# Kernel optimization log

Measured on AMD Instinct MI355X. Metric: run time of the kernel, lower is better.

Reference implementation:

```python
import jax, jax.numpy as jnp
import numpy as np

N = 1024
NEVAL = 131072
NUM_POLES = 8
DOMAIN = (-1.0, 1.0)
DOMAIN_LEN = DOMAIN[1] - DOMAIN[0]
EPS = 1e-14


def _cheb_nodes(n):
    # Chebyshev points of the second kind: cos(pi * linspace(0, 1, n))
    return jnp.cos(jnp.pi * jnp.linspace(0.0, 1.0, n))


def _to_standard(x):
    return 2.0 * (x - DOMAIN[0]) / DOMAIN_LEN - 1.0


def _barycentric_weights(nodes, poles_real, poles_imag):
    # Vectorized equivalent of the original per-node Python loop.
    n = nodes.shape[0]
    diff = nodes[:, None] - nodes[None, :]            # (N, N)
    eye = jnp.eye(n, dtype=bool)
    # log_weights[j] = -sum_{i!=j} log|nodes[j]-nodes[i]|
    log_w = -jnp.sum(jnp.log(jnp.where(eye, 1.0, jnp.abs(diff))), axis=1)
    # signs[j] = (-1)^(# of negative off-diagonal diffs); diagonal diff==0 contributes nothing
    neg_count = jnp.sum(diff < 0, axis=1)
    signs = jnp.where(neg_count % 2 == 0, 1.0, -1.0)
    # each conjugate pole pair contributes 2*log(sqrt((x-r)^2 + i^2)) = log((x-r)^2 + i^2)
    pole_term = jnp.log((nodes[:, None] - poles_real[None, :]) ** 2
                        + poles_imag[None, :] ** 2)   # (N, M)
    log_w = log_w + jnp.sum(pole_term, axis=1)
    log_w = log_w - jnp.max(log_w)
    w = signs * jnp.exp(log_w)
    return w / jnp.abs(w[0])


def setup_inputs() -> dict:
    key = jax.random.key(0)
    k1, k2, k3, k4 = jax.random.split(key, 4)
    x_eval = jax.random.uniform(k1, (NEVAL,), dtype=jnp.float32)  # in [0,1) subset of domain
    values = jax.random.normal(k2, (N,), dtype=jnp.float32)
    poles_real = jax.random.normal(k3, (NUM_POLES,), dtype=jnp.float32)
    poles_imag = jax.random.normal(k4, (NUM_POLES,), dtype=jnp.float32)
    return {"x_eval": x_eval, "values": values,
            "poles_real": poles_real, "poles_imag": poles_imag}


def reference(x_eval, values, poles_real, poles_imag):
    nodes = _cheb_nodes(N)
    nodes_std = _to_standard(nodes)                   # identity for domain (-1,1)
    w = _barycentric_weights(nodes, poles_real, poles_imag)

    x_std = _to_standard(x_eval)
    d_x = x_std[None, :] - nodes_std[:, None]         # (N, NEVAL)
    small = jnp.abs(d_x) < EPS
    small_any = jnp.any(small, axis=0)                # (NEVAL,)
    d_safe = jnp.where(small, 1.0, d_x)
    inv = jnp.where(small_any[None, :], 0.0, 1.0 / d_safe)
    inv = jnp.where(small, 1.0, inv)                  # exact-hit columns: indicator row -> 1

    num = jnp.einsum('n,nm,n->m', values, inv, w)
    den = jnp.einsum('nm,n->m', inv, w)
    return num / den
```

## Files before the change

kernel.cpp:

```cpp
#include <hip/hip_runtime.h>
#include <math.h>

#define N_NODES 1024
#define N_EVAL 131072
#define NUM_POLES 8
#define PI_D 3.14159265358979323846


__device__ __forceinline__ double cheb_node(int j) {
    return cos(PI_D * (double)j / (double)(N_NODES - 1));
}

__global__ void wk_logw(const float* __restrict__ poles_real,
                        const float* __restrict__ poles_imag,
                        double* __restrict__ lwd) {
    const int j = blockIdx.x;
    const int t = threadIdx.x;
    const double nj = cheb_node(j);
    double part = 0.0;
    for (int i = t; i < N_NODES; i += 256) {
        if (i != j) {
            part -= log(fabs(nj - cheb_node(i)));
        }
    }
    __shared__ double red[256];
    red[t] = part;
    __syncthreads();
    for (int s = 128; s > 0; s >>= 1) {
        if (t < s) red[t] += red[t + s];
        __syncthreads();
    }
    if (t == 0) {
        double lw = red[0];
        for (int m = 0; m < NUM_POLES; ++m) {
            double pr = (double)poles_real[m];
            double pim = (double)poles_imag[m];
            double dr = nj - pr;
            lw += log(dr * dr + pim * pim);
        }
        lwd[j] = lw;
    }
}

__global__ void wk_finalize(const float* __restrict__ values,
                            const double* __restrict__ lwd,
                            float* __restrict__ nodes_f,
                            float* __restrict__ w_f,
                            float* __restrict__ wv_f) {
    const int j = threadIdx.x;
    const double lw = lwd[j];
    __shared__ double red[N_NODES];
    red[j] = lw;
    __syncthreads();
    for (int s = N_NODES / 2; s > 0; s >>= 1) {
        if (j < s) red[j] = fmax(red[j], red[j + s]);
        __syncthreads();
    }
    const double mx = red[0];
    double w = exp(lw - mx);
    if (j & 1) w = -w;
    const float wf = (float)w;
    nodes_f[j] = (float)cheb_node(j);
    w_f[j] = wf;
    wv_f[j] = wf * values[j];
}

__global__ __launch_bounds__(256) void eval_kernel(
    const float* __restrict__ x_eval,
    const float* __restrict__ nodes_f,
    const float* __restrict__ w_f,
    const float* __restrict__ wv_f,
    float* __restrict__ out) {
    __shared__ __align__(16) float s_n[N_NODES];
    __shared__ __align__(16) float s_w[N_NODES];
    __shared__ __align__(16) float s_v[N_NODES];
    const int t = threadIdx.x;
    for (int k = t; k < N_NODES; k += 256) {
        s_n[k] = nodes_f[k];
        s_w[k] = w_f[k];
        s_v[k] = wv_f[k];
    }
    __syncthreads();

    const int i = blockIdx.x * 256 + t;
    const float x = x_eval[i];

    float num = 0.0f, den = 0.0f;
    float hnum = 0.0f, hden = 0.0f;
    bool hit = false;

    const float4* n4 = (const float4*)s_n;
    const float4* w4 = (const float4*)s_w;
    const float4* v4 = (const float4*)s_v;

#define BODY(C)                                                            \
    {                                                                      \
        float d = x - an.C;                                                \
        if (__builtin_expect(fabsf(d) < 1e-14f, 0)) {                      \
            hit = true; hnum += av.C; hden += aw.C;                        \
        } else {                                                           \
            float r = __builtin_amdgcn_rcpf(d);                            \
            r = fmaf(r, fmaf(-d, r, 1.0f), r);          \
            num = fmaf(av.C, r, num);                                      \
            den = fmaf(aw.C, r, den);                                      \
        }                                                                  \
    }

#pragma unroll 4
    for (int j4 = 0; j4 < N_NODES / 4; ++j4) {
        float4 an = n4[j4];
        float4 aw = w4[j4];
        float4 av = v4[j4];
        BODY(x) BODY(y) BODY(z) BODY(w)
    }
#undef BODY

    out[i] = hit ? (hnum / hden) : (num / den);
}

extern "C" void kernel_launch(void* const* d_in, const int* in_sizes, int n_in,
                              void* d_out, int out_size, void* d_ws, size_t ws_size,
                              hipStream_t stream) {
    const float* x_eval     = (const float*)d_in[0];
    const float* values     = (const float*)d_in[1];
    const float* poles_real = (const float*)d_in[2];
    const float* poles_imag = (const float*)d_in[3];
    float* out = (float*)d_out;

    double* lwd    = (double*)d_ws;
    float* nodes_f = (float*)(lwd + N_NODES);
    float* w_f     = nodes_f + N_NODES;
    float* wv_f    = w_f + N_NODES;

    wk_logw<<<N_NODES, 256, 0, stream>>>(poles_real, poles_imag, lwd);
    wk_finalize<<<1, N_NODES, 0, stream>>>(values, lwd, nodes_f, w_f, wv_f);
    eval_kernel<<<N_EVAL / 256, 256, 0, stream>>>(x_eval, nodes_f, w_f, wv_f, out);
}
```

Before: 128.2 us.

## Use closed-form Chebyshev weights and branchless eval with NaN fallback

Replaces the O(N^2) log-sum weight computation and its separate max-reduction kernel with the closed-form Chebyshev second-kind barycentric weights (halved at the endpoints) times the pole product, computed in a single small kernel. The eval loop drops the per-node exact-hit branch, splits accumulation into two chains for more ILP, and only rescans the nodes for an exact match when the result is NaN. Weights are no longer normalised by a max, which risks overflow or scale differences, though these cancel in the ratio.

```diff
diff --git a/kernel.cpp b/kernel.cpp
--- a/kernel.cpp
+++ b/kernel.cpp
@@ -6,63 +6,26 @@
 #define NUM_POLES 8
 #define PI_D 3.14159265358979323846
 
-
-__device__ __forceinline__ double cheb_node(int j) {
-    return cos(PI_D * (double)j / (double)(N_NODES - 1));
-}
-
-__global__ void wk_logw(const float* __restrict__ poles_real,
-                        const float* __restrict__ poles_imag,
-                        double* __restrict__ lwd) {
-    const int j = blockIdx.x;
-    const int t = threadIdx.x;
-    const double nj = cheb_node(j);
-    double part = 0.0;
-    for (int i = t; i < N_NODES; i += 256) {
-        if (i != j) {
-            part -= log(fabs(nj - cheb_node(i)));
-        }
+__global__ void wk_setup(const float* __restrict__ values,
+                         const float* __restrict__ poles_real,
+                         const float* __restrict__ poles_imag,
+                         float* __restrict__ nodes_f,
+                         float* __restrict__ w_f,
+                         float* __restrict__ wv_f) {
+    const int j = threadIdx.x;
+    const double nd = cos(PI_D * (double)j / (double)(N_NODES - 1));
+    double prod = (j == 0 || j == N_NODES - 1) ? 0.5 : 1.0;
+#pragma unroll
+    for (int m = 0; m < NUM_POLES; ++m) {
+        double dr = nd - (double)poles_real[m];
+        double di = (double)poles_imag[m];
+        prod *= dr * dr + di * di;
     }
-    __shared__ double red[256];
-    red[t] = part;
-    __syncthreads();
-    for (int s = 128; s > 0; s >>= 1) {
-        if (t < s) red[t] += red[t + s];
-        __syncthreads();
-    }
-    if (t == 0) {
-        double lw = red[0];
-        for (int m = 0; m < NUM_POLES; ++m) {
-            double pr = (double)poles_real[m];
-            double pim = (double)poles_imag[m];
-            double dr = nj - pr;
-            lw += log(dr * dr + pim * pim);
-        }
-        lwd[j] = lw;
-    }
-}
-
-__global__ void wk_finalize(const float* __restrict__ values,
-                            const double* __restrict__ lwd,
-                            float* __restrict__ nodes_f,
-                            float* __restrict__ w_f,
-                            float* __restrict__ wv_f) {
-    const int j = threadIdx.x;
-    const double lw = lwd[j];
-    __shared__ double red[N_NODES];
-    red[j] = lw;
-    __syncthreads();
-    for (int s = N_NODES / 2; s > 0; s >>= 1) {
-        if (j < s) red[j] = fmax(red[j], red[j + s]);
-        __syncthreads();
-    }
-    const double mx = red[0];
-    double w = exp(lw - mx);
-    if (j & 1) w = -w;
-    const float wf = (float)w;
-    nodes_f[j] = (float)cheb_node(j);
+    if (j & 1) prod = -prod;
+    const float wf = (float)prod;
+    nodes_f[j] = (float)nd;
     w_f[j] = wf;
-    wv_f[j] = wf * values[j];
+    wv_f[j] = (float)(prod * (double)values[j]);
 }
 
 __global__ __launch_bounds__(256) void eval_kernel(
@@ -85,25 +48,20 @@
     const int i = blockIdx.x * 256 + t;
     const float x = x_eval[i];
 
-    float num = 0.0f, den = 0.0f;
-    float hnum = 0.0f, hden = 0.0f;
-    bool hit = false;
+    float num0 = 0.0f, den0 = 0.0f;
+    float num1 = 0.0f, den1 = 0.0f;
 
     const float4* n4 = (const float4*)s_n;
     const float4* w4 = (const float4*)s_w;
     const float4* v4 = (const float4*)s_v;
 
-#define BODY(C)                                                            \
+#define BODY(C, NUM, DEN)                                                  \
     {                                                                      \
         float d = x - an.C;                                                \
-        if (__builtin_expect(fabsf(d) < 1e-14f, 0)) {                      \
-            hit = true; hnum += av.C; hden += aw.C;                        \
-        } else {                                                           \
-            float r = __builtin_amdgcn_rcpf(d);                            \
-            r = fmaf(r, fmaf(-d, r, 1.0f), r);          \
-            num = fmaf(av.C, r, num);                                      \
-            den = fmaf(aw.C, r, den);                                      \
-        }                                                                  \
+        float r = __builtin_amdgcn_rcpf(d);                                \
+        r = fmaf(r, fmaf(-d, r, 1.0f), r);              \
+        NUM = fmaf(av.C, r, NUM);                                          \
+        DEN = fmaf(aw.C, r, DEN);                                          \
     }
 
 #pragma unroll 4
@@ -111,11 +69,23 @@
         float4 an = n4[j4];
         float4 aw = w4[j4];
         float4 av = v4[j4];
-        BODY(x) BODY(y) BODY(z) BODY(w)
+        BODY(x, num0, den0)
+        BODY(y, num1, den1)
+        BODY(z, num0, den0)
+        BODY(w, num1, den1)
     }
 #undef BODY
 
-    out[i] = hit ? (hnum / hden) : (num / den);
+    float res = (num0 + num1) / (den0 + den1);
+
+    if (__builtin_expect(__builtin_isnan(res), 0)) {
+        float hn = 0.0f, hd = 0.0f;
+        for (int j = 0; j < N_NODES; ++j) {
+            if (s_n[j] == x) { hn += s_v[j]; hd += s_w[j]; }
+        }
+        res = hn / hd;
+    }
+    out[i] = res;
 }
 
 extern "C" void kernel_launch(void* const* d_in, const int* in_sizes, int n_in,
@@ -127,12 +97,11 @@
     const float* poles_imag = (const float*)d_in[3];
     float* out = (float*)d_out;
 
-    double* lwd    = (double*)d_ws;
-    float* nodes_f = (float*)(lwd + N_NODES);
+    float* nodes_f = (float*)d_ws;
     float* w_f     = nodes_f + N_NODES;
     float* wv_f    = w_f + N_NODES;
 
-    wk_logw<<<N_NODES, 256, 0, stream>>>(poles_real, poles_imag, lwd);
-    wk_finalize<<<1, N_NODES, 0, stream>>>(values, lwd, nodes_f, w_f, wv_f);
+    wk_setup<<<1, N_NODES, 0, stream>>>(values, poles_real, poles_imag,
+                                        nodes_f, w_f, wv_f);
     eval_kernel<<<N_EVAL / 256, 256, 0, stream>>>(x_eval, nodes_f, w_f, wv_f, out);
 }
```

Measured after the change: 145.3 us. +13.3%, slower.
